# Performance work log

Hardware: AMD Instinct MI355X
Metric: run time of the kernel (lower is better)

Reference implementation:

```python
import jax, jax.numpy as jnp
import numpy as np

B, N, E, HID, H = 4, 16384, 131072, 128, 8
D = HID // H


def layer_norm(x, g, b, eps=1e-5):
    m = jnp.mean(x, axis=-1, keepdims=True)
    v = jnp.var(x, axis=-1, keepdims=True)
    return (x - m) * jax.lax.rsqrt(v + eps) * g + b


def setup_inputs() -> dict:
    key = jax.random.key(0)
    ks = jax.random.split(key, 16)
    s = 0.05
    return {
        "h": jax.random.normal(ks[0], (B, N, HID), jnp.float32),
        "edge_features_raw": jax.random.uniform(ks[1], (B, E, 2), jnp.float32),
        "edge_index": jax.random.randint(ks[2], (B, 2, E), 0, N),
        "n_edges": jax.random.randint(ks[3], (B, 1), 0, E),
        "Wq": jax.random.normal(ks[4], (HID, HID), jnp.float32) * s,
        "Wk": jax.random.normal(ks[5], (HID, HID), jnp.float32) * s,
        "Wv": jax.random.normal(ks[6], (HID, HID), jnp.float32) * s,
        "Wo": jax.random.normal(ks[7], (HID, HID), jnp.float32) * s,
        "bo": jnp.zeros((HID,), jnp.float32),
        "We": jax.random.normal(ks[8], (2, H), jnp.float32) * s,
        "ln1_g": jnp.ones((HID,), jnp.float32),
        "ln1_b": jnp.zeros((HID,), jnp.float32),
        "ln2_g": jnp.ones((HID,), jnp.float32),
        "ln2_b": jnp.zeros((HID,), jnp.float32),
        "ff1": jax.random.normal(ks[9], (HID, 2 * HID), jnp.float32) * s,
        "b1": jnp.zeros((2 * HID,), jnp.float32),
        "ff2": jax.random.normal(ks[10], (2 * HID, HID), jnp.float32) * s,
        "b2": jnp.zeros((HID,), jnp.float32),
    }


def reference(h, edge_features_raw, edge_index, n_edges, Wq, Wk, Wv, Wo, bo, We,
              ln1_g, ln1_b, ln2_g, ln2_b, ff1, b1, ff2, b2):
    Bd, Nd, HIDd = h.shape
    Ed = edge_index.shape[2]
    src = edge_index[:, 0, :]  # (B, E)
    dst = edge_index[:, 1, :]  # (B, E)

    Q = (h @ Wq).reshape(Bd, Nd, H, D)
    K = (h @ Wk).reshape(Bd, Nd, H, D)
    V = (h @ Wv).reshape(Bd, Nd, H, D)

    # edge gathers: Q by dst (query node), K/V by src (as in the source)
    Q_edge = jnp.take_along_axis(Q, dst[:, :, None, None], axis=1)  # (B,E,H,D)
    K_edge = jnp.take_along_axis(K, src[:, :, None, None], axis=1)
    V_edge = jnp.take_along_axis(V, src[:, :, None, None], axis=1)

    scale = D ** (-0.5)
    logits = jnp.einsum('behd,behd->beh', Q_edge, K_edge) * scale
    logits = logits + edge_features_raw @ We  # (B,E,H)

    edge_mask = jnp.arange(Ed)[None, :] < n_edges  # (B,E)
    logits = jnp.where(edge_mask[:, :, None], logits, -jnp.inf)

    def segment_attend(lg, Ve, d, mb):
        # lg (E,H), Ve (E,H,D), d (E,), mb (E,)
        node_max = jnp.full((Nd, H), -jnp.inf, lg.dtype).at[d].max(lg)
        node_max = jnp.maximum(node_max, -1e9)
        p = jnp.exp(lg - node_max[d]) * mb[:, None].astype(lg.dtype)
        denom = jnp.zeros((Nd, H), lg.dtype).at[d].add(p)
        alpha = p / jnp.maximum(denom[d], 1e-6)
        return jnp.zeros((Nd, H, D), lg.dtype).at[d].add(alpha[:, :, None] * Ve)

    out = jax.vmap(segment_attend)(logits, V_edge, dst, edge_mask)  # (B,N,H,D)
    out = out.reshape(Bd, Nd, HIDd) @ Wo + bo

    h = layer_norm(h + out, ln1_g, ln1_b)
    ff = jax.nn.relu(h @ ff1 + b1) @ ff2 + b2
    h = layer_norm(h + ff, ln2_g, ln2_b)
    return h
```

## Files before the change

### kernel.cpp

```cpp
#include <hip/hip_runtime.h>
#include <string.h>

constexpr int Bc   = 4;
constexpr int Nc   = 16384;
constexpr int Ec   = 131072;
constexpr int Hc   = 8;
constexpr int Dc   = 16;
constexpr int HIDc = 128;
constexpr int BN   = Bc * Nc;
constexpr int CAP  = 32;


typedef __bf16 bf16_t;
typedef bf16_t bf16x8 __attribute__((ext_vector_type(8)));
typedef float  f32x4  __attribute__((ext_vector_type(4)));

typedef uint4    uint4_a  __attribute__((may_alias));
typedef unsigned uint_a   __attribute__((may_alias));
typedef float2   float2_a __attribute__((may_alias));
typedef float4   float4_a __attribute__((may_alias));

union BF8 { bf16x8 v; uint4 u; unsigned short s[8]; };

__device__ inline float b2f(unsigned short u) {
    return __uint_as_float(((unsigned)u) << 16);
}
__device__ inline unsigned short f2b(float f) {
    unsigned b = __float_as_uint(f);
    unsigned r = (b + 0x7FFFu + ((b >> 16) & 1u)) >> 16;
    return (unsigned short)r;
}
__device__ inline float lo16(unsigned u) { return __uint_as_float(u << 16); }
__device__ inline float hi16(unsigned u) { return __uint_as_float(u & 0xFFFF0000u); }

__device__ inline void gll16(const void* g, void* l) {
    __builtin_amdgcn_global_load_lds(
        (const __attribute__((address_space(1))) void*)g,
        (__attribute__((address_space(3))) void*)l, 16, 0, 0);
}

__global__ __launch_bounds__(1024) void k_prep(const float* __restrict__ Wq,
                                               const float* __restrict__ Wk,
                                               const float* __restrict__ Wv,
                                               const float* __restrict__ Wo,
                                               const float* __restrict__ ff1,
                                               const float* __restrict__ ff2,
                                               unsigned short* __restrict__ wbuf,
                                               unsigned* __restrict__ counts) {
    if (blockIdx.x >= 7) {
        int i = (blockIdx.x - 7) * 1024 + threadIdx.x;
        counts[i] = 0u;
        return;
    }
    int t = blockIdx.x;
    const float* W;
    int pitch, col0, chunks;
    size_t off = (size_t)t * 16384;
    switch (t) {
        case 0: W = Wq;  pitch = 128; col0 = 0;   chunks = 16; break;
        case 1: W = Wk;  pitch = 128; col0 = 0;   chunks = 16; break;
        case 2: W = Wv;  pitch = 128; col0 = 0;   chunks = 16; break;
        case 3: W = Wo;  pitch = 128; col0 = 0;   chunks = 16; break;
        case 4: W = ff1; pitch = 256; col0 = 0;   chunks = 16; break;
        case 5: W = ff1; pitch = 256; col0 = 128; chunks = 16; break;
        default: W = ff2; pitch = 128; col0 = 0;  chunks = 32; break;
    }
    const int KD = chunks * 8;
    for (int idx = threadIdx.x; idx < 128 * chunks; idx += 1024) {
        int n = idx & 127;
        int c = idx >> 7;
        BF8 pk;
#pragma unroll
        for (int j = 0; j < 8; ++j)
            pk.v[j] = (bf16_t)W[(size_t)(c * 8 + j) * pitch + col0 + n];
        *(uint4_a*)&wbuf[off + (size_t)n * KD + (c ^ (n & 7)) * 8] = pk.u;
    }
}

__global__ __launch_bounds__(256) void k_fill2(const int* __restrict__ eidx,
                                               const int* __restrict__ nedges,
                                               const float* __restrict__ ef,
                                               unsigned* __restrict__ counts,
                                               uint4* __restrict__ csr2) {
    int t = blockIdx.x * 256 + threadIdx.x;
    int b = t >> 17;
    int e = t & (Ec - 1);
    if (e >= nedges[b]) return;
    int dst = eidx[(size_t)(b * 2 + 1) * Ec + e];
    int src = eidx[(size_t)(b * 2 + 0) * Ec + e];
    float2 f = *(const float2_a*)(ef + ((size_t)b * Ec + e) * 2);
    unsigned node = (unsigned)(b * Nc + dst);
    unsigned slot = atomicAdd(&counts[node], 1u);
    if (slot < (unsigned)CAP)
        csr2[(size_t)node * CAP + slot] =
            make_uint4((unsigned)src, __float_as_uint(f.x), __float_as_uint(f.y), 0u);
}

__global__ __launch_bounds__(256) void k_qkv3(const float* __restrict__ h,
                                              const unsigned short* __restrict__ wbuf,
                                              unsigned short* __restrict__ Q,
                                              unsigned short* __restrict__ K,
                                              unsigned short* __restrict__ V) {
    __shared__ __attribute__((aligned(16))) unsigned short wt[16384];
    const int wave = threadIdx.x >> 6, lane = threadIdx.x & 63;
    const int nn = lane & 15, q = lane >> 4;
    const int row0 = blockIdx.x * 64 + wave * 16;

    bf16x8 afrag[4];
    {
        const float* A = h + (size_t)(row0 + nn) * 128;
#pragma unroll
        for (int ks = 0; ks < 4; ++ks) {
            int k0 = ks * 32 + q * 8;
            float4 f0 = *(const float4_a*)(A + k0);
            float4 f1 = *(const float4_a*)(A + k0 + 4);
            BF8 pk;
            pk.v[0] = (bf16_t)f0.x; pk.v[1] = (bf16_t)f0.y;
            pk.v[2] = (bf16_t)f0.z; pk.v[3] = (bf16_t)f0.w;
            pk.v[4] = (bf16_t)f1.x; pk.v[5] = (bf16_t)f1.y;
            pk.v[6] = (bf16_t)f1.z; pk.v[7] = (bf16_t)f1.w;
            afrag[ks] = pk.v;
        }
    }

#pragma unroll 1
    for (int s = 0; s < 3; ++s) {
        unsigned short* O = (s == 0) ? Q : ((s == 1) ? K : V);
        if (s) __syncthreads();
        {
            const uint4* src = (const uint4*)(wbuf + (size_t)s * 16384);
            uint4* dst = (uint4*)wt;
            for (int i = threadIdx.x; i < 2048; i += 256)
                gll16(src + i, dst + i);
        }
        __syncthreads();
        f32x4 acc[8];
#pragma unroll
        for (int nt = 0; nt < 8; ++nt) acc[nt] = (f32x4){0.f, 0.f, 0.f, 0.f};
#pragma unroll
        for (int nt = 0; nt < 8; ++nt) {
            int n = nt * 16 + nn;
#pragma unroll
            for (int ks = 0; ks < 4; ++ks) {
                int c = ks * 4 + q;
                BF8 bf;
                bf.u = *(const uint4_a*)&wt[n * 128 + (c ^ (n & 7)) * 8];
                acc[nt] = __builtin_amdgcn_mfma_f32_16x16x32_bf16(
                    afrag[ks], bf.v, acc[nt], 0, 0, 0);
            }
        }
#pragma unroll
        for (int nt = 0; nt < 8; ++nt) {
            int col = nt * 16 + nn;
#pragma unroll
            for (int r = 0; r < 4; ++r)
                O[(size_t)(row0 + q * 4 + r) * 128 + col] = f2b(acc[nt][r]);
        }
    }
}

__global__ __launch_bounds__(256) void k_attn(const unsigned short* __restrict__ Q,
                                              const unsigned short* __restrict__ K,
                                              const unsigned short* __restrict__ V,
                                              const unsigned* __restrict__ counts,
                                              const uint4* __restrict__ csr2,
                                              const float* __restrict__ We,
                                              unsigned short* __restrict__ attn) {
    int wave = threadIdx.x >> 6, lane = threadIdx.x & 63;
    int i = blockIdx.x * 4 + wave;
    int b = i >> 14;
    int hh = lane >> 3;
    int j  = lane & 7;
    int col = hh * 16 + j * 2;

    unsigned qv = *(const uint_a*)(Q + (size_t)i * 128 + col);
    float q0 = lo16(qv), q1 = hi16(qv);
    float we0 = We[hh], we1 = We[8 + hh];

    unsigned deg = counts[i];
    if (deg > (unsigned)CAP) deg = CAP;
    const uint4* bkt = csr2 + (size_t)i * CAP;
    const unsigned short* Kb = K + (size_t)b * Nc * 128;
    const unsigned short* Vb = V + (size_t)b * Nc * 128;

    float m = -INFINITY, l = 0.f, a0 = 0.f, a1 = 0.f;
    unsigned p = 0;
    for (; p + 4 <= deg; p += 4) {
        uint4 t4[4]; unsigned kv[4], vv[4];
#pragma unroll
        for (int u = 0; u < 4; ++u) t4[u] = bkt[p + u];
#pragma unroll
        for (int u = 0; u < 4; ++u) {
            kv[u] = *(const uint_a*)(Kb + (size_t)t4[u].x * 128 + col);
            vv[u] = *(const uint_a*)(Vb + (size_t)t4[u].x * 128 + col);
        }
        float lg[4];
#pragma unroll
        for (int u = 0; u < 4; ++u) {
            float d = q0 * lo16(kv[u]) + q1 * hi16(kv[u]);
            d += __shfl_xor(d, 1, 64);
            d += __shfl_xor(d, 2, 64);
            d += __shfl_xor(d, 4, 64);
            lg[u] = 0.25f * d + __uint_as_float(t4[u].y) * we0
                              + __uint_as_float(t4[u].z) * we1;
        }
        float M = fmaxf(fmaxf(fmaxf(lg[0], lg[1]), fmaxf(lg[2], lg[3])), m);
        float sc = __expf(m - M);
        float pr[4];
#pragma unroll
        for (int u = 0; u < 4; ++u) pr[u] = __expf(lg[u] - M);
        l  = l * sc + ((pr[0] + pr[1]) + (pr[2] + pr[3]));
        a0 = a0 * sc + pr[0] * lo16(vv[0]) + pr[1] * lo16(vv[1])
                     + pr[2] * lo16(vv[2]) + pr[3] * lo16(vv[3]);
        a1 = a1 * sc + pr[0] * hi16(vv[0]) + pr[1] * hi16(vv[1])
                     + pr[2] * hi16(vv[2]) + pr[3] * hi16(vv[3]);
        m = M;
    }
    for (; p < deg; ++p) {
        uint4 t1 = bkt[p];
        unsigned kv = *(const uint_a*)(Kb + (size_t)t1.x * 128 + col);
        unsigned vv = *(const uint_a*)(Vb + (size_t)t1.x * 128 + col);
        float d = q0 * lo16(kv) + q1 * hi16(kv);
        d += __shfl_xor(d, 1, 64);
        d += __shfl_xor(d, 2, 64);
        d += __shfl_xor(d, 4, 64);
        float lg = 0.25f * d + __uint_as_float(t1.y) * we0
                             + __uint_as_float(t1.z) * we1;
        float nm = fmaxf(m, lg);
        float sc = __expf(m - nm);
        float pr = __expf(lg - nm);
        l  = l * sc + pr;
        a0 = a0 * sc + pr * lo16(vv);
        a1 = a1 * sc + pr * hi16(vv);
        m = nm;
    }
    float rcp = 1.f / fmaxf(l, 1e-6f);
    unsigned pack = (unsigned)f2b(a0 * rcp) | ((unsigned)f2b(a1 * rcp) << 16);
    *(uint_a*)(attn + (size_t)i * 128 + col) = pack;
}

constexpr int H1P  = 136;
constexpr int MIDP = 264;

__global__ __launch_bounds__(256) void k_mlp(const unsigned short* __restrict__ attn,
                                             const float* __restrict__ h,
                                             const unsigned short* __restrict__ wbuf,
                                             const float* __restrict__ bo,
                                             const float* __restrict__ ln1g,
                                             const float* __restrict__ ln1b,
                                             const float* __restrict__ b1,
                                             const float* __restrict__ b2,
                                             const float* __restrict__ ln2g,
                                             const float* __restrict__ ln2b,
                                             float* __restrict__ out) {
    __shared__ __attribute__((aligned(16))) unsigned short wLDS[32768];
    __shared__ __attribute__((aligned(16))) unsigned short hT[4 * 16 * H1P];
    __shared__ __attribute__((aligned(16))) unsigned short midT[4 * 16 * MIDP];

    const int wave = threadIdx.x >> 6, lane = threadIdx.x & 63;
    const int nn = lane & 15, q = lane >> 4;
    const int rowbase = blockIdx.x * 64 + wave * 16;
    unsigned short* hTw   = hT   + wave * 16 * H1P;
    unsigned short* midTw = midT + wave * 16 * MIDP;

    {
        const uint4* src = (const uint4*)(wbuf + 3 * 16384);
        uint4* dst = (uint4*)wLDS;
        for (int i = threadIdx.x; i < 2048; i += 256)
            gll16(src + i, dst + i);
    }
    bf16x8 af0[4];
    {
        const unsigned short* A = attn + (size_t)(rowbase + nn) * 128;
#pragma unroll
        for (int ks = 0; ks < 4; ++ks) {
            BF8 pk;
            pk.u = *(const uint4_a*)(A + ks * 32 + q * 8);
            af0[ks] = pk.v;
        }
    }
    float res[8][4];
#pragma unroll
    for (int nt = 0; nt < 8; ++nt)
#pragma unroll
        for (int r = 0; r < 4; ++r)
            res[nt][r] = h[(size_t)(rowbase + q * 4 + r) * 128 + nt * 16 + nn];
    __syncthreads();

    f32x4 acc[8];
#pragma unroll
    for (int nt = 0; nt < 8; ++nt) acc[nt] = (f32x4){0.f, 0.f, 0.f, 0.f};
#pragma unroll
    for (int nt = 0; nt < 8; ++nt) {
        int n = nt * 16 + nn;
#pragma unroll
        for (int ks = 0; ks < 4; ++ks) {
            int c = ks * 4 + q;
            BF8 bf;
            bf.u = *(const uint4_a*)&wLDS[n * 128 + (c ^ (n & 7)) * 8];
            acc[nt] = __builtin_amdgcn_mfma_f32_16x16x32_bf16(af0[ks], bf.v,
                                                              acc[nt], 0, 0, 0);
        }
    }

    float h1v[8][4];
    {
        float rs[4] = {0, 0, 0, 0}, rq[4] = {0, 0, 0, 0};
#pragma unroll
        for (int nt = 0; nt < 8; ++nt) {
            float bv = bo[nt * 16 + nn];
#pragma unroll
            for (int r = 0; r < 4; ++r) {
                float x = acc[nt][r] + bv + res[nt][r];
                h1v[nt][r] = x;
                rs[r] += x; rq[r] += x * x;
            }
        }
#pragma unroll
        for (int r = 0; r < 4; ++r) {
#pragma unroll
            for (int o = 1; o < 16; o <<= 1) {
                rs[r] += __shfl_xor(rs[r], o, 64);
                rq[r] += __shfl_xor(rq[r], o, 64);
            }
        }
#pragma unroll
        for (int r = 0; r < 4; ++r) {
            float mean = rs[r] * (1.f / 128.f);
            float var  = rq[r] * (1.f / 128.f) - mean * mean;
            float rstd = rsqrtf(var + 1e-5f);
#pragma unroll
            for (int nt = 0; nt < 8; ++nt) {
                int col = nt * 16 + nn;
                h1v[nt][r] = (h1v[nt][r] - mean) * rstd * ln1g[col] + ln1b[col];
            }
        }
    }
#pragma unroll
    for (int nt = 0; nt < 8; ++nt)
#pragma unroll
        for (int r = 0; r < 4; ++r)
            hTw[(q * 4 + r) * H1P + nt * 16 + nn] = f2b(h1v[nt][r]);

    __syncthreads();
    {
        const uint4* src = (const uint4*)(wbuf + 4 * 16384);
        uint4* dst = (uint4*)wLDS;
        for (int i = threadIdx.x; i < 4096; i += 256)
            gll16(src + i, dst + i);
    }
    __syncthreads();

    bf16x8 af1[4];
#pragma unroll
    for (int ks = 0; ks < 4; ++ks) {
        BF8 pk;
        pk.u = *(const uint4_a*)&hTw[nn * H1P + ks * 32 + q * 8];
        af1[ks] = pk.v;
    }
    f32x4 acc1[16];
#pragma unroll
    for (int nt = 0; nt < 16; ++nt) acc1[nt] = (f32x4){0.f, 0.f, 0.f, 0.f};
#pragma unroll
    for (int nt = 0; nt < 16; ++nt) {
        const unsigned short* wb = wLDS + (nt >> 3) * 16384 + ((nt & 7) * 16 + nn) * 128;
#pragma unroll
        for (int ks = 0; ks < 4; ++ks) {
            int c = ks * 4 + q;
            BF8 bf;
            bf.u = *(const uint4_a*)&wb[(c ^ (nn & 7)) * 8];
            acc1[nt] = __builtin_amdgcn_mfma_f32_16x16x32_bf16(af1[ks], bf.v,
                                                               acc1[nt], 0, 0, 0);
        }
    }
#pragma unroll
    for (int nt = 0; nt < 16; ++nt) {
        int col = nt * 16 + nn;
        float bv = b1[col];
#pragma unroll
        for (int r = 0; r < 4; ++r)
            midTw[(q * 4 + r) * MIDP + col] = f2b(fmaxf(acc1[nt][r] + bv, 0.f));
    }

    __syncthreads();
    {
        const uint4* src = (const uint4*)(wbuf + 6 * 16384);
        uint4* dst = (uint4*)wLDS;
        for (int i = threadIdx.x; i < 4096; i += 256)
            gll16(src + i, dst + i);
    }
    __syncthreads();

    bf16x8 af2[8];
#pragma unroll
    for (int ks = 0; ks < 8; ++ks) {
        BF8 pk;
        pk.u = *(const uint4_a*)&midTw[nn * MIDP + ks * 32 + q * 8];
        af2[ks] = pk.v;
    }
    f32x4 acc2[8];
#pragma unroll
    for (int nt = 0; nt < 8; ++nt) acc2[nt] = (f32x4){0.f, 0.f, 0.f, 0.f};
#pragma unroll
    for (int nt = 0; nt < 8; ++nt) {
        int n = nt * 16 + nn;
#pragma unroll
        for (int ks = 0; ks < 8; ++ks) {
            int c = ks * 4 + q;
            BF8 bf;
            bf.u = *(const uint4_a*)&wLDS[n * 256 + (c ^ (n & 7)) * 8];
            acc2[nt] = __builtin_amdgcn_mfma_f32_16x16x32_bf16(af2[ks], bf.v,
                                                               acc2[nt], 0, 0, 0);
        }
    }
    {
        float rs[4] = {0, 0, 0, 0}, rq[4] = {0, 0, 0, 0};
#pragma unroll
        for (int nt = 0; nt < 8; ++nt) {
            float bv = b2[nt * 16 + nn];
#pragma unroll
            for (int r = 0; r < 4; ++r) {
                float x = acc2[nt][r] + bv + h1v[nt][r];
                acc2[nt][r] = x;
                rs[r] += x; rq[r] += x * x;
            }
        }
#pragma unroll
        for (int r = 0; r < 4; ++r) {
#pragma unroll
            for (int o = 1; o < 16; o <<= 1) {
                rs[r] += __shfl_xor(rs[r], o, 64);
                rq[r] += __shfl_xor(rq[r], o, 64);
            }
        }
#pragma unroll
        for (int r = 0; r < 4; ++r) {
            float mean = rs[r] * (1.f / 128.f);
            float var  = rq[r] * (1.f / 128.f) - mean * mean;
            float rstd = rsqrtf(var + 1e-5f);
            int row = rowbase + q * 4 + r;
#pragma unroll
            for (int nt = 0; nt < 8; ++nt) {
                int col = nt * 16 + nn;
                out[(size_t)row * 128 + col] =
                    (acc2[nt][r] - mean) * rstd * ln2g[col] + ln2b[col];
            }
        }
    }
}

extern "C" void kernel_launch(void* const* d_in, const int* in_sizes, int n_in,
                              void* d_out, int out_size, void* d_ws, size_t ws_size,
                              hipStream_t stream) {
    const float* h    = (const float*)d_in[0];
    const float* ef   = (const float*)d_in[1];
    const int*   eidx = (const int*)d_in[2];
    const int*   ne   = (const int*)d_in[3];
    const float* Wq   = (const float*)d_in[4];
    const float* Wk   = (const float*)d_in[5];
    const float* Wv   = (const float*)d_in[6];
    const float* Wo   = (const float*)d_in[7];
    const float* bo   = (const float*)d_in[8];
    const float* We   = (const float*)d_in[9];
    const float* ln1g = (const float*)d_in[10];
    const float* ln1b = (const float*)d_in[11];
    const float* ln2g = (const float*)d_in[12];
    const float* ln2b = (const float*)d_in[13];
    const float* ff1  = (const float*)d_in[14];
    const float* b1   = (const float*)d_in[15];
    const float* ff2  = (const float*)d_in[16];
    const float* b2   = (const float*)d_in[17];

    constexpr size_t MB = 1024 * 1024;
    char* ws = (char*)d_ws;
    unsigned short* Q      = (unsigned short*)(ws + 0 * MB);
    unsigned short* Kp     = (unsigned short*)(ws + 16 * MB);
    unsigned short* V      = (unsigned short*)(ws + 32 * MB);
    unsigned short* attn   = (unsigned short*)(ws + 48 * MB);
    unsigned*       counts = (unsigned*)(ws + 64 * MB);
    unsigned short* wbuf   = (unsigned short*)(ws + 65 * MB);
    uint4*          csr2   = (uint4*)(ws + 66 * MB);

    const int edgeBlocks = (Bc * Ec) / 256;
    const int qkvBlocks  = BN / 64;
    const int mlpBlocks  = BN / 64;

    k_prep<<<71, 1024, 0, stream>>>(Wq, Wk, Wv, Wo, ff1, ff2, wbuf, counts);
    k_fill2<<<edgeBlocks, 256, 0, stream>>>(eidx, ne, ef, counts, csr2);
    k_qkv3<<<qkvBlocks, 256, 0, stream>>>(h, wbuf, Q, Kp, V);
    k_attn<<<BN / 4, 256, 0, stream>>>(Q, Kp, V, counts, csr2, We, attn);
    k_mlp<<<mlpBlocks, 256, 0, stream>>>(attn, h, wbuf, bo, ln1g, ln1b,
                                         b1, b2, ln2g, ln2b, (float*)d_out);
}
```

Baseline: 241.5 us.

## Double MLP block rows to amortize weight staging and swizzle staging buffers

The fused MLP kernel now runs 512 threads (8 waves) per block covering 128 rows instead of 64, so each weight matrix staged into LDS is reused by twice as many rows and total weight reload traffic halves. The padded hT/midT staging buffers are replaced with unpadded XOR-swizzled layouts to avoid LDS bank conflicts without padding. LDS per block grows (64KB weights plus larger staging), which may reduce blocks per CU and occupancy.

```diff
diff --git a/kernel.cpp b/kernel.cpp
--- a/kernel.cpp
+++ b/kernel.cpp
@@ -239,10 +239,7 @@
     *(uint_a*)(attn + (size_t)i * 128 + col) = pack;
 }
 
-constexpr int H1P  = 136;
-constexpr int MIDP = 264;
-
-__global__ __launch_bounds__(256) void k_mlp(const unsigned short* __restrict__ attn,
+__global__ __launch_bounds__(512) void k_mlp(const unsigned short* __restrict__ attn,
                                              const float* __restrict__ h,
                                              const unsigned short* __restrict__ wbuf,
                                              const float* __restrict__ bo,
@@ -254,19 +251,19 @@
                                              const float* __restrict__ ln2b,
                                              float* __restrict__ out) {
     __shared__ __attribute__((aligned(16))) unsigned short wLDS[32768];
-    __shared__ __attribute__((aligned(16))) unsigned short hT[4 * 16 * H1P];
-    __shared__ __attribute__((aligned(16))) unsigned short midT[4 * 16 * MIDP];
+    __shared__ __attribute__((aligned(16))) unsigned short hT[8 * 16 * 128];
+    __shared__ __attribute__((aligned(16))) unsigned short midT[8 * 16 * 256];
 
     const int wave = threadIdx.x >> 6, lane = threadIdx.x & 63;
     const int nn = lane & 15, q = lane >> 4;
-    const int rowbase = blockIdx.x * 64 + wave * 16;
-    unsigned short* hTw   = hT   + wave * 16 * H1P;
-    unsigned short* midTw = midT + wave * 16 * MIDP;
+    const int rowbase = blockIdx.x * 128 + wave * 16;
+    unsigned short* hTw   = hT   + wave * 2048;
+    unsigned short* midTw = midT + wave * 4096;
 
     {
         const uint4* src = (const uint4*)(wbuf + 3 * 16384);
         uint4* dst = (uint4*)wLDS;
-        for (int i = threadIdx.x; i < 2048; i += 256)
+        for (int i = threadIdx.x; i < 2048; i += 512)
             gll16(src + i, dst + i);
     }
     bf16x8 af0[4];
@@ -339,14 +336,17 @@
 #pragma unroll
     for (int nt = 0; nt < 8; ++nt)
 #pragma unroll
-        for (int r = 0; r < 4; ++r)
-            hTw[(q * 4 + r) * H1P + nt * 16 + nn] = f2b(h1v[nt][r]);
+        for (int r = 0; r < 4; ++r) {
+            int row = q * 4 + r, col = nt * 16 + nn;
+            hTw[row * 128 + (((col >> 3) ^ (row & 7)) << 3) + (col & 7)] =
+                f2b(h1v[nt][r]);
+        }
 
     __syncthreads();
     {
         const uint4* src = (const uint4*)(wbuf + 4 * 16384);
         uint4* dst = (uint4*)wLDS;
-        for (int i = threadIdx.x; i < 4096; i += 256)
+        for (int i = threadIdx.x; i < 4096; i += 512)
             gll16(src + i, dst + i);
     }
     __syncthreads();
@@ -354,8 +354,9 @@
     bf16x8 af1[4];
 #pragma unroll
     for (int ks = 0; ks < 4; ++ks) {
+        int c = ks * 4 + q;
         BF8 pk;
-        pk.u = *(const uint4_a*)&hTw[nn * H1P + ks * 32 + q * 8];
+        pk.u = *(const uint4_a*)&hTw[nn * 128 + ((c ^ (nn & 7)) << 3)];
         af1[ks] = pk.v;
     }
     f32x4 acc1[16];
@@ -378,15 +379,18 @@
         int col = nt * 16 + nn;
         float bv = b1[col];
 #pragma unroll
-        for (int r = 0; r < 4; ++r)
-            midTw[(q * 4 + r) * MIDP + col] = f2b(fmaxf(acc1[nt][r] + bv, 0.f));
+        for (int r = 0; r < 4; ++r) {
+            int row = q * 4 + r;
+            midTw[row * 256 + (((col >> 3) ^ (row & 7)) << 3) + (col & 7)] =
+                f2b(fmaxf(acc1[nt][r] + bv, 0.f));
+        }
     }
 
     __syncthreads();
     {
         const uint4* src = (const uint4*)(wbuf + 6 * 16384);
         uint4* dst = (uint4*)wLDS;
-        for (int i = threadIdx.x; i < 4096; i += 256)
+        for (int i = threadIdx.x; i < 4096; i += 512)
             gll16(src + i, dst + i);
     }
     __syncthreads();
@@ -394,8 +398,9 @@
     bf16x8 af2[8];
 #pragma unroll
     for (int ks = 0; ks < 8; ++ks) {
+        int c = ks * 4 + q;
         BF8 pk;
-        pk.u = *(const uint4_a*)&midTw[nn * MIDP + ks * 32 + q * 8];
+        pk.u = *(const uint4_a*)&midTw[nn * 256 + ((c ^ (nn & 7)) << 3)];
         af2[ks] = pk.v;
     }
     f32x4 acc2[8];
@@ -483,12 +488,12 @@
 
     const int edgeBlocks = (Bc * Ec) / 256;
     const int qkvBlocks  = BN / 64;
-    const int mlpBlocks  = BN / 64;
+    const int mlpBlocks  = BN / 128;
 
     k_prep<<<71, 1024, 0, stream>>>(Wq, Wk, Wv, Wo, ff1, ff2, wbuf, counts);
     k_fill2<<<edgeBlocks, 256, 0, stream>>>(eidx, ne, ef, counts, csr2);
     k_qkv3<<<qkvBlocks, 256, 0, stream>>>(h, wbuf, Q, Kp, V);
     k_attn<<<BN / 4, 256, 0, stream>>>(Q, Kp, V, counts, csr2, We, attn);
-    k_mlp<<<mlpBlocks, 256, 0, stream>>>(attn, h, wbuf, bo, ln1g, ln1b,
+    k_mlp<<<mlpBlocks, 512, 0, stream>>>(attn, h, wbuf, bo, ln1g, ln1b,
                                          b1, b2, ln2g, ln2b, (float*)d_out);
 }
```

After: 227.1 us. 6.0% less time.
